# Kernel tuning notes

Hardware: AMD Instinct MI355X
Metric: run time of the kernel (lower is better)

The kernel has to match this reference:

```python
import jax, jax.numpy as jnp
import numpy as np

N_NODES = 4096
N_EDGES = 500000
N_PAIRS = 2000000
EDGE_DIM = 16
MAX_PATH = 5


def setup_inputs() -> dict:
    key = jax.random.key(0)
    k1, k2, k3, k4, k5 = jax.random.split(key, 5)
    x = jax.random.normal(k1, (N_NODES, EDGE_DIM), dtype=jnp.float32)
    edge_attr = jax.random.normal(k2, (N_EDGES, EDGE_DIM), dtype=jnp.float32)
    path_idx = jax.random.randint(k3, (N_PAIRS, MAX_PATH), 0, N_EDGES, dtype=jnp.int64)
    path_lens = jax.random.randint(k4, (N_PAIRS,), 0, MAX_PATH + 1, dtype=jnp.int64)
    pair_id = jnp.arange(N_PAIRS, dtype=jnp.int64)
    # learned parameter: edge_weights [max_path_distance, edge_dim]
    edge_weights = jax.random.normal(k5, (MAX_PATH, EDGE_DIM), dtype=jnp.float32)
    return {"x": x, "edge_attr": edge_attr, "edge_weights": edge_weights,
            "path_idx": path_idx, "path_lens": path_lens, "pair_id": pair_id}


def reference(x, edge_attr, edge_weights, path_idx, path_lens, pair_id):
    N = x.shape[0]
    L = edge_weights.shape[0]  # max_path_distance
    # valid-position mask for each ragged path, padded to length L
    mask = (jnp.arange(L)[None, :] < path_lens[:, None]).astype(edge_attr.dtype)  # [P, L]
    gathered = edge_attr[path_idx]  # [P, L, D] ragged gather of edge features
    # per-hop dot with learned per-hop weight vector, i.e. (w_l * e_l).sum(dim=1)
    dots = jnp.einsum('pld,ld->pl', gathered, edge_weights)  # [P, L]
    s = jnp.sum(dots * mask, axis=1)  # [P]
    cnt = path_lens.astype(edge_attr.dtype)
    # mean over valid hops; empty path -> NaN in torch -> nan_to_num -> 0
    mean = jnp.where(cnt > 0, s / jnp.maximum(cnt, 1.0), jnp.zeros_like(s))
    src = pair_id % N
    dst = pair_id // N  # unique (src, dst) pairs by construction
    cij = jnp.zeros((N, N), dtype=edge_attr.dtype).at[src, dst].set(mean)
    return cij
```

## Files before the change

### kernel.cpp

```cpp
#include <hip/hip_runtime.h>
#include <hip/hip_fp16.h>

#define NNODES 4096
#define NEDGES 500000
#define NPAIRS 2000000
#define EDIM   16
#define LMAX   5

typedef int v4i __attribute__((ext_vector_type(4)));
typedef float v4f __attribute__((ext_vector_type(4)));

__device__ __forceinline__ v4i ntload4(const int* p) {
  return __builtin_nontemporal_load((const v4i*)p);
}
__device__ __forceinline__ void ntstore4(float* p, float x, float y, float z, float w) {
  v4f t = {x, y, z, w};
  __builtin_nontemporal_store(t, (v4f*)p);
}

__global__ __launch_bounds__(256) void dots_kernel(
    const float* __restrict__ edge_attr,
    const float* __restrict__ ew,
    __half* __restrict__ dots) {
  __shared__ float w[LMAX * EDIM];
  int tid = threadIdx.x;
  if (tid < LMAX * EDIM) w[tid] = ew[tid];
  __syncthreads();

  int e0 = (blockIdx.x * 256 + tid) * 2;
  if (e0 >= NEDGES) return;

  const float4* ra = (const float4*)(edge_attr + (size_t)e0 * EDIM);
  float4 a0 = ra[0], a1 = ra[1], a2 = ra[2], a3 = ra[3];
  float4 b0 = ra[4], b1 = ra[5], b2 = ra[6], b3 = ra[7];
  float va[16] = {a0.x, a0.y, a0.z, a0.w, a1.x, a1.y, a1.z, a1.w,
                  a2.x, a2.y, a2.z, a2.w, a3.x, a3.y, a3.z, a3.w};
  float vb[16] = {b0.x, b0.y, b0.z, b0.w, b1.x, b1.y, b1.z, b1.w,
                  b2.x, b2.y, b2.z, b2.w, b3.x, b3.y, b3.z, b3.w};
#pragma unroll
  for (int l = 0; l < LMAX; ++l) {
    float da = 0.f, db = 0.f;
#pragma unroll
    for (int k = 0; k < EDIM; ++k) {
      da += va[k] * w[l * EDIM + k];
      db += vb[k] * w[l * EDIM + k];
    }
    __half2 h;
    h.x = __float2half(da);
    h.y = __float2half(db);
    *(__half2*)(dots + (size_t)l * NEDGES + e0) = h;
  }
}

__device__ __forceinline__ float pair_mean(
    const __half* __restrict__ dots, int len,
    int i0, int i1, int i2, int i3, int i4) {
  len = min(max(len, 0), LMAX);
  float v0 = (len > 0) ? __half2float(dots[i0]) : 0.f;
  float v1 = (len > 1) ? __half2float(dots[1 * NEDGES + i1]) : 0.f;
  float v2 = (len > 2) ? __half2float(dots[2 * NEDGES + i2]) : 0.f;
  float v3 = (len > 3) ? __half2float(dots[3 * NEDGES + i3]) : 0.f;
  float v4 = (len > 4) ? __half2float(dots[4 * NEDGES + i4]) : 0.f;
  float s = ((v0 + v1) + (v2 + v3)) + v4;
  return (len > 0) ? s / (float)len : 0.f;
}

__global__ __launch_bounds__(1024) void fused_mean_transpose(
    const int* __restrict__ path_idx,
    const int* __restrict__ path_lens,
    const __half* __restrict__ dots,
    float* __restrict__ out) {
  int bid = blockIdx.x;
  int dst_t, src_t;
  bool heavy;
  if (bid < 1024) {
    heavy = (bid & 1);
    int k = bid >> 1;
    if (heavy) { dst_t = k & 7;        src_t = k >> 3; }
    else       { dst_t = 8 + (k >> 6); src_t = k & 63; }
  } else {
    heavy = false;
    int z = bid - 512;
    dst_t = 8 + (z >> 6);
    src_t = z & 63;
  }
  const int src0 = src_t * 64;
  const int dst0 = dst_t * 64;
  const int tid = threadIdx.x;
  const int a = tid >> 4;
  const int c = tid & 15;

  if (!heavy) {
    ntstore4(out + (size_t)(src0 + a) * NNODES + dst0 + 4 * c, 0.f, 0.f, 0.f, 0.f);
    return;
  }

  __shared__ float tile[64][65];

  {
    int p = (dst0 + a) * NNODES + src0 + 4 * c;
    float4 v = {0.f, 0.f, 0.f, 0.f};
    if (p < NPAIRS) {
      v4i ln = ntload4(path_lens + p);
      const int* q = path_idx + (size_t)p * LMAX;
      v4i A = ntload4(q);
      v4i B = ntload4(q + 4);
      v4i C = ntload4(q + 8);
      v4i D = ntload4(q + 12);
      v4i E = ntload4(q + 16);
      v.x = pair_mean(dots, ln[0], A[0], A[1], A[2], A[3], B[0]);
      v.y = pair_mean(dots, ln[1], B[1], B[2], B[3], C[0], C[1]);
      v.z = pair_mean(dots, ln[2], C[2], C[3], D[0], D[1], D[2]);
      v.w = pair_mean(dots, ln[3], D[3], E[0], E[1], E[2], E[3]);
    }
    tile[a][4 * c + 0] = v.x;
    tile[a][4 * c + 1] = v.y;
    tile[a][4 * c + 2] = v.z;
    tile[a][4 * c + 3] = v.w;
  }
  __syncthreads();
  {
    float x = tile[4 * c + 0][a];
    float y = tile[4 * c + 1][a];
    float z = tile[4 * c + 2][a];
    float w = tile[4 * c + 3][a];
    ntstore4(out + (size_t)(src0 + a) * NNODES + dst0 + 4 * c, x, y, z, w);
  }
}

__global__ __launch_bounds__(256) void scatter_kernel(
    const float* __restrict__ edge_attr,
    const float* __restrict__ ew,
    const int* __restrict__ path_idx,
    const int* __restrict__ path_lens,
    float* __restrict__ out) {
  __shared__ float w[LMAX * EDIM];
  if (threadIdx.x < LMAX * EDIM) w[threadIdx.x] = ew[threadIdx.x];
  __syncthreads();

  int p = blockIdx.x * 256 + threadIdx.x;
  if (p >= NPAIRS) return;

  int len = path_lens[p];
  len = min(max(len, 0), LMAX);

  const int* row = path_idx + (size_t)p * LMAX;
  float s = 0.f;
  for (int l = 0; l < len; ++l) {
    int idx = row[l];
    const float4* r = (const float4*)(edge_attr + (size_t)idx * EDIM);
    float4 a0 = r[0], a1 = r[1], a2 = r[2], a3 = r[3];
    const float* wl = &w[l * EDIM];
    s += a0.x * wl[0] + a0.y * wl[1] + a0.z * wl[2] + a0.w * wl[3] +
         a1.x * wl[4] + a1.y * wl[5] + a1.z * wl[6] + a1.w * wl[7] +
         a2.x * wl[8] + a2.y * wl[9] + a2.z * wl[10] + a2.w * wl[11] +
         a3.x * wl[12] + a3.y * wl[13] + a3.z * wl[14] + a3.w * wl[15];
  }
  float m = (len > 0) ? (s / (float)len) : 0.f;
  int src = p & (NNODES - 1);
  int dst = p >> 12;
  out[(size_t)src * NNODES + dst] = m;
}

extern "C" void kernel_launch(void* const* d_in, const int* in_sizes, int n_in,
                              void* d_out, int out_size, void* d_ws, size_t ws_size,
                              hipStream_t stream) {
  const float* edge_attr = (const float*)d_in[1];
  const float* edge_w    = (const float*)d_in[2];
  const int*   path_idx  = (const int*)d_in[3];
  const int*   path_lens = (const int*)d_in[4];
  float* out = (float*)d_out;

  const size_t need = (size_t)LMAX * NEDGES * sizeof(__half);

  if (ws_size >= need) {
    __half* dots = (__half*)d_ws;

    dots_kernel<<<(NEDGES / 2 + 255) / 256, 256, 0, stream>>>(edge_attr, edge_w, dots);
    fused_mean_transpose<<<4096, 1024, 0, stream>>>(path_idx, path_lens, dots, out);
  } else {
    hipMemsetAsync(d_out, 0, (size_t)out_size * sizeof(float), stream);
    scatter_kernel<<<(NPAIRS + 255) / 256, 256, 0, stream>>>(
        edge_attr, edge_w, path_idx, path_lens, out);
  }
}
```

Baseline: 217.2 us.

## Split transpose into 256-thread blocks and make dot gathers unconditional

The fused mean+transpose kernel moves from 1024-thread blocks covering 64x64 tiles to 256-thread blocks covering 64x16 sub-tiles for the heavy region, with launch bounds asking for 8 blocks per CU. Zero-fill blocks now each write a full 64x64 tile with four stores per thread, and heavy blocks are grouped first rather than interleaved. The five dot gathers in pair_mean are now issued unconditionally and masked afterwards, so loads can be in flight together without branches, at the cost of extra memory traffic for short paths. The shared-memory tile is written transposed and read row-wise, which changes the LDS bank pattern.

```diff
diff --git a/kernel.cpp b/kernel.cpp
--- a/kernel.cpp
+++ b/kernel.cpp
@@ -56,49 +56,52 @@
     const __half* __restrict__ dots, int len,
     int i0, int i1, int i2, int i3, int i4) {
   len = min(max(len, 0), LMAX);
-  float v0 = (len > 0) ? __half2float(dots[i0]) : 0.f;
-  float v1 = (len > 1) ? __half2float(dots[1 * NEDGES + i1]) : 0.f;
-  float v2 = (len > 2) ? __half2float(dots[2 * NEDGES + i2]) : 0.f;
-  float v3 = (len > 3) ? __half2float(dots[3 * NEDGES + i3]) : 0.f;
-  float v4 = (len > 4) ? __half2float(dots[4 * NEDGES + i4]) : 0.f;
-  float s = ((v0 + v1) + (v2 + v3)) + v4;
+  float v0 = __half2float(dots[i0]);
+  float v1 = __half2float(dots[1 * NEDGES + i1]);
+  float v2 = __half2float(dots[2 * NEDGES + i2]);
+  float v3 = __half2float(dots[3 * NEDGES + i3]);
+  float v4 = __half2float(dots[4 * NEDGES + i4]);
+  float s = ((len > 0 ? v0 : 0.f) + (len > 1 ? v1 : 0.f)) +
+            ((len > 2 ? v2 : 0.f) + (len > 3 ? v3 : 0.f)) +
+            (len > 4 ? v4 : 0.f);
   return (len > 0) ? s / (float)len : 0.f;
 }
 
-__global__ __launch_bounds__(1024) void fused_mean_transpose(
+#define NHEAVY 2048
+
+__global__ __launch_bounds__(256, 8) void fused_mean_transpose(
     const int* __restrict__ path_idx,
     const int* __restrict__ path_lens,
     const __half* __restrict__ dots,
     float* __restrict__ out) {
-  int bid = blockIdx.x;
-  int dst_t, src_t;
-  bool heavy;
-  if (bid < 1024) {
-    heavy = (bid & 1);
-    int k = bid >> 1;
-    if (heavy) { dst_t = k & 7;        src_t = k >> 3; }
-    else       { dst_t = 8 + (k >> 6); src_t = k & 63; }
-  } else {
-    heavy = false;
-    int z = bid - 512;
-    dst_t = 8 + (z >> 6);
-    src_t = z & 63;
-  }
-  const int src0 = src_t * 64;
-  const int dst0 = dst_t * 64;
+  const int bid = blockIdx.x;
   const int tid = threadIdx.x;
-  const int a = tid >> 4;
-  const int c = tid & 15;
 
-  if (!heavy) {
-    ntstore4(out + (size_t)(src0 + a) * NNODES + dst0 + 4 * c, 0.f, 0.f, 0.f, 0.f);
+  if (bid >= NHEAVY) {
+    int z = bid - NHEAVY;
+    int dst0 = (8 + (z >> 6)) * 64;
+    int src0 = (z & 63) * 64;
+#pragma unroll
+    for (int i = 0; i < 4; ++i) {
+      int slot = tid + i * 256;
+      int a = slot >> 4;
+      int c = slot & 15;
+      ntstore4(out + (size_t)(src0 + a) * NNODES + dst0 + 4 * c, 0.f, 0.f, 0.f, 0.f);
+    }
     return;
   }
 
-  __shared__ float tile[64][65];
+  const int t = bid >> 2;
+  const int s = bid & 3;
+  const int dst0 = (t & 7) * 64;
+  const int srcc0 = (t >> 3) * 64 + s * 16;
+
+  __shared__ float tile[16][65];
 
   {
-    int p = (dst0 + a) * NNODES + src0 + 4 * c;
+    const int a = tid >> 2;
+    const int c = tid & 3;
+    int p = (dst0 + a) * NNODES + srcc0 + 4 * c;
     float4 v = {0.f, 0.f, 0.f, 0.f};
     if (p < NPAIRS) {
       v4i ln = ntload4(path_lens + p);
@@ -113,18 +116,20 @@
       v.z = pair_mean(dots, ln[2], C[2], C[3], D[0], D[1], D[2]);
       v.w = pair_mean(dots, ln[3], D[3], E[0], E[1], E[2], E[3]);
     }
-    tile[a][4 * c + 0] = v.x;
-    tile[a][4 * c + 1] = v.y;
-    tile[a][4 * c + 2] = v.z;
-    tile[a][4 * c + 3] = v.w;
+    tile[4 * c + 0][a] = v.x;
+    tile[4 * c + 1][a] = v.y;
+    tile[4 * c + 2][a] = v.z;
+    tile[4 * c + 3][a] = v.w;
   }
   __syncthreads();
   {
-    float x = tile[4 * c + 0][a];
-    float y = tile[4 * c + 1][a];
-    float z = tile[4 * c + 2][a];
-    float w = tile[4 * c + 3][a];
-    ntstore4(out + (size_t)(src0 + a) * NNODES + dst0 + 4 * c, x, y, z, w);
+    const int r = tid >> 4;
+    const int c = tid & 15;
+    float x = tile[r][4 * c + 0];
+    float y = tile[r][4 * c + 1];
+    float z = tile[r][4 * c + 2];
+    float w = tile[r][4 * c + 3];
+    ntstore4(out + (size_t)(srcc0 + r) * NNODES + dst0 + 4 * c, x, y, z, w);
   }
 }
 
@@ -177,7 +182,7 @@
     __half* dots = (__half*)d_ws;
 
     dots_kernel<<<(NEDGES / 2 + 255) / 256, 256, 0, stream>>>(edge_attr, edge_w, dots);
-    fused_mean_transpose<<<4096, 1024, 0, stream>>>(path_idx, path_lens, dots, out);
+    fused_mean_transpose<<<NHEAVY + 3584, 256, 0, stream>>>(path_idx, path_lens, dots, out);
   } else {
     hipMemsetAsync(d_out, 0, (size_t)out_size * sizeof(float), stream);
     scatter_kernel<<<(NPAIRS + 255) / 256, 256, 0, stream>>>(
```

After: 196.4 us. 9.6% less time.
